# Optimization experiments

Measured on AMD Instinct MI355X. Metric: run time of the kernel, lower is better.

The kernel has to match this reference:

```python
import jax, jax.numpy as jnp
import numpy as np

B, N, C, H = 4, 128, 512, 8
D = C // H
SCALE = D ** (-0.5) * 50.0


def setup_inputs() -> dict:
    key = jax.random.key(0)
    kx, kw = jax.random.split(key)
    x = jax.random.normal(kx, (B, N, N, C), dtype=jnp.float32)
    # torch Linear(n_embd, 5*n_embd, bias=False); stored here as [in, out] for x @ w
    w_qkv = jax.random.normal(kw, (C, 5 * C), dtype=jnp.float32) * (C ** -0.5)
    return {"x": x, "w_qkv": w_qkv}


def _heads(t):
    # [b, i, j, h*d] -> [b, h, i, j, d]
    b, i, j, _ = t.shape
    return t.reshape(b, i, j, H, D).transpose(0, 3, 1, 2, 4)


def reference(x, w_qkv):
    # global norm over the entire tensor (torch .std() is unbiased, ddof=1)
    x = (x - x.mean()) / x.std(ddof=1)
    qkv = x @ w_qkv                                   # [b, i, j, 5c]
    q, k1, k2, v1, v2 = map(_heads, jnp.split(qkv, 5, axis=-1))
    # pivotal attention: for query (i,j), pivot over k with row stream k1[i,k]
    # and column stream k2[k,j]
    scores = SCALE * (jnp.einsum('bhijd,bhikd->bhijk', q, k1)
                      + jnp.einsum('bhijd,bhkjd->bhijk', q, k2))
    attn = jax.nn.softmax(scores, axis=-1)            # [b, h, i, j, k]
    out = (jnp.einsum('bhijk,bhikd->bhijd', attn, v1)
           + jnp.einsum('bhijk,bhkjd->bhijd', attn, v2))
    # [b, h, i, j, d] -> [b, i, j, h*d]
    return out.transpose(0, 2, 3, 1, 4).reshape(B, N, N, C)
```

## Files before the change

### kernel.cpp

```cpp
#include <hip/hip_runtime.h>
#include <stdint.h>


typedef __attribute__((ext_vector_type(8))) short s8v;
typedef __attribute__((ext_vector_type(4))) float f4v;

#define MFMA(a, b, c) __builtin_amdgcn_mfma_f32_16x16x32_bf16((a), (b), (c), 0, 0, 0)

__device__ __forceinline__ float bf2f(unsigned short u) {
  union { unsigned int i; float f; } v; v.i = ((unsigned int)u) << 16; return v.f;
}
__device__ __forceinline__ unsigned short f2bf(float f) {
  union { float f; unsigned int i; } v; v.f = f;
  unsigned int i = v.i;
  return (unsigned short)((i + 0x7fffu + ((i >> 16) & 1u)) >> 16);
}

__device__ __forceinline__ void async_copy16(const void* g, void* l) {
  __builtin_amdgcn_global_load_lds(
      (const __attribute__((address_space(1))) unsigned int*)(uintptr_t)g,
      (__attribute__((address_space(3))) unsigned int*)(uintptr_t)l,
      16, 0, 0);
}

__global__ __launch_bounds__(256) void k_probe(const unsigned short* __restrict__ x,
                                               int* __restrict__ flag) {
  uint4 v = ((const uint4*)x)[threadIdx.x];
  unsigned int uu[4] = {v.x, v.y, v.z, v.w};
  int bad = 0;
#pragma unroll
  for (int u = 0; u < 4; ++u) {
    float a = bf2f((unsigned short)(uu[u] & 0xffffu));
    float b = bf2f((unsigned short)(uu[u] >> 16));
    if (!(fabsf(a) <= 1e4f)) bad = 1;
    if (!(fabsf(b) <= 1e4f)) bad = 1;
  }
  if (bad) atomicOr(flag, 1);
}

__global__ __launch_bounds__(256) void k_red(const void* __restrict__ xraw,
                                             const int* __restrict__ flag,
                                             double* __restrict__ dstats) {
  __shared__ float red[8];
  const int fm = flag[0];
  int t = threadIdx.x;
  size_t gid = (size_t)blockIdx.x * 256 + t;
  float s = 0.f, ss = 0.f;
  if (fm) {
    const float4* pf = (const float4*)xraw;
#pragma unroll 4
    for (int it = 0; it < 32; ++it) {
      size_t idx = gid + (size_t)it * 131072;
      float4 u1 = pf[2 * idx], u2 = pf[2 * idx + 1];
      float vals[8] = {u1.x, u1.y, u1.z, u1.w, u2.x, u2.y, u2.z, u2.w};
#pragma unroll
      for (int u = 0; u < 8; ++u) { s += vals[u]; ss += vals[u] * vals[u]; }
    }
  } else {
    const uint4* p = (const uint4*)xraw;
#pragma unroll 4
    for (int it = 0; it < 32; ++it) {
      uint4 v = p[gid + (size_t)it * 131072];
      unsigned int uu[4] = {v.x, v.y, v.z, v.w};
#pragma unroll
      for (int u = 0; u < 4; ++u) {
        float a = bf2f((unsigned short)(uu[u] & 0xffffu));
        float b = bf2f((unsigned short)(uu[u] >> 16));
        s += a + b;
        ss += a * a + b * b;
      }
    }
  }
#pragma unroll
  for (int d = 32; d >= 1; d >>= 1) {
    s += __shfl_down(s, d);
    ss += __shfl_down(ss, d);
  }
  int lane = t & 63, wave = t >> 6;
  if (lane == 0) { red[wave] = s; red[4 + wave] = ss; }
  __syncthreads();
  if (t == 0) {
    atomicAdd(&dstats[0], (double)(red[0] + red[1] + red[2] + red[3]));
    atomicAdd(&dstats[1], (double)(red[4] + red[5] + red[6] + red[7]));
  }
}

__global__ void k_stats(const double* __restrict__ dstats, float* __restrict__ fstats) {
  double M = 33554432.0;
  double mean = dstats[0] / M;
  double var = (dstats[1] - dstats[0] * dstats[0] / M) / (M - 1.0);
  double istd = 1.0 / sqrt(var);
  fstats[0] = (float)istd;
  fstats[1] = (float)(-mean * istd);
}

__global__ __launch_bounds__(256) void k_colsum(const void* __restrict__ wraw,
                                                const int* __restrict__ flag,
                                                float* __restrict__ colsum) {
  const int fm = flag[0];
  int c = blockIdx.x * 256 + threadIdx.x;
  if (c >= 2560) return;
  float s = 0.f;
  if (fm) {
    const float* w = (const float*)wraw;
    for (int r = 0; r < 512; ++r) s += w[(size_t)r * 2560 + c];
  } else {
    const unsigned short* w = (const unsigned short*)wraw;
    for (int r = 0; r < 512; ++r) s += bf2f(w[(size_t)r * 2560 + c]);
  }
  colsum[c] = s;
}

__global__ __launch_bounds__(256) void k_wt(const void* __restrict__ wraw,
                                            const int* __restrict__ flag,
                                            unsigned short* __restrict__ wThi,
                                            unsigned short* __restrict__ wTlo) {
  __shared__ float tile[64][65];
  const int fm = flag[0];
  int n0 = blockIdx.x * 64, r0 = blockIdx.y * 64;
#pragma unroll
  for (int rep = 0; rep < 16; ++rep) {
    int idx = rep * 256 + threadIdx.x;
    int r = idx >> 6, n = idx & 63;
    float v;
    if (fm) v = ((const float*)wraw)[(size_t)(r0 + r) * 2560 + n0 + n];
    else    v = bf2f(((const unsigned short*)wraw)[(size_t)(r0 + r) * 2560 + n0 + n]);
    tile[r][n] = v;
  }
  __syncthreads();
#pragma unroll
  for (int rep = 0; rep < 16; ++rep) {
    int idx = rep * 256 + threadIdx.x;
    int n = idx >> 6, r = idx & 63;
    float v = tile[r][n];
    unsigned short hi = f2bf(v);
    size_t o = (size_t)(n0 + n) * 512 + r0 + r;
    wThi[o] = hi;
    wTlo[o] = f2bf(v - bf2f(hi));
  }
}

__global__ __launch_bounds__(256) void k_convx(const void* __restrict__ xraw,
                                               const int* __restrict__ flag,
                                               unsigned short* __restrict__ xhi,
                                               unsigned short* __restrict__ xlo,
                                               int b) {
  const int fm = flag[0];
  size_t e0 = ((size_t)blockIdx.x * 256 + threadIdx.x) * 8;
  size_t g0 = (size_t)b * 8388608 + e0;
  float vals[8];
  if (fm) {
    const float4* pf = (const float4*)xraw;
    float4 u1 = pf[g0 / 4], u2 = pf[g0 / 4 + 1];
    vals[0] = u1.x; vals[1] = u1.y; vals[2] = u1.z; vals[3] = u1.w;
    vals[4] = u2.x; vals[5] = u2.y; vals[6] = u2.z; vals[7] = u2.w;
  } else {
    uint4 v = ((const uint4*)xraw)[g0 / 8];
    unsigned int uu[4] = {v.x, v.y, v.z, v.w};
#pragma unroll
    for (int u = 0; u < 4; ++u) {
      vals[2 * u] = bf2f((unsigned short)(uu[u] & 0xffffu));
      vals[2 * u + 1] = bf2f((unsigned short)(uu[u] >> 16));
    }
  }
  unsigned short h[8], l[8];
#pragma unroll
  for (int u = 0; u < 8; ++u) {
    h[u] = f2bf(vals[u]);
    l[u] = f2bf(vals[u] - bf2f(h[u]));
  }
  *(uint4*)(xhi + e0) = *(const uint4*)h;
  *(uint4*)(xlo + e0) = *(const uint4*)l;
}

__global__ __launch_bounds__(256) void k_gemm(
    const unsigned short* __restrict__ xhi, const unsigned short* __restrict__ xlo,
    const unsigned short* __restrict__ wThi, const unsigned short* __restrict__ wTlo,
    const float* __restrict__ colsum, const float* __restrict__ fstats,
    const int* __restrict__ flag,
    unsigned short* __restrict__ qhi, unsigned short* __restrict__ qlo,
    unsigned short* __restrict__ k1hi, unsigned short* __restrict__ k1lo,
    unsigned short* __restrict__ k2hi, unsigned short* __restrict__ k2lo,
    unsigned short* __restrict__ v1T, unsigned short* __restrict__ v2T,
    int h0, int hcShift) {
  __shared__ __align__(16) unsigned short Ash[128 * 64];
  __shared__ __align__(16) unsigned short Asl[128 * 64];
  __shared__ __align__(16) unsigned short Bsh[128 * 64];
  __shared__ __align__(16) unsigned short Bsl[128 * 64];
  const int fm = flag[0];
  const int t = threadIdx.x;
  const int m0 = blockIdx.x * 128;
  const int n0 = blockIdx.y * 128;
  const int hcMask = (1 << hcShift) - 1;

  const int lane = t & 63, wave = t >> 6;
  const int wm = (wave & 1) * 64, wn = (wave >> 1) * 64;
  const int l16 = lane & 15, q4 = lane >> 4;
  const int srow = t >> 3;
  const int scol = (((t & 7) ^ ((t >> 3) & 7)) * 8);
  const int rsw = l16 & 7;

  const float af = fstats[0], bfc = fstats[1];
  const unsigned short* xh = xhi + (size_t)m0 * 512;
  const unsigned short* xl = xlo + (size_t)m0 * 512;

  int wcolr[4];
#pragma unroll
  for (int r = 0; r < 4; ++r) {
    int ncol = n0 + r * 32 + srow;
    int g = ncol >> hcShift, rem = ncol & hcMask;
    wcolr[r] = (g << 9) + ((h0 + (rem >> 6)) << 6) + (rem & 63);
  }

  f4v acc[4][4];
#pragma unroll
  for (int a = 0; a < 4; ++a)
#pragma unroll
    for (int c = 0; c < 4; ++c) acc[a][c] = (f4v)0.f;

  for (int k0 = 0; k0 < 512; k0 += 64) {
#pragma unroll
    for (int r = 0; r < 4; ++r) {
      int row = r * 32 + srow;
      async_copy16(xh + (size_t)row * 512 + k0 + scol, (char*)Ash + (r * 256 + t) * 16);
    }
#pragma unroll
    for (int r = 0; r < 4; ++r)
      async_copy16(wThi + (size_t)wcolr[r] * 512 + k0 + scol, (char*)Bsh + (r * 256 + t) * 16);
    if (fm) {
#pragma unroll
      for (int r = 0; r < 4; ++r) {
        int row = r * 32 + srow;
        async_copy16(xl + (size_t)row * 512 + k0 + scol, (char*)Asl + (r * 256 + t) * 16);
      }
#pragma unroll
      for (int r = 0; r < 4; ++r)
        async_copy16(wTlo + (size_t)wcolr[r] * 512 + k0 + scol, (char*)Bsl + (r * 256 + t) * 16);
    }
    __syncthreads();
#pragma unroll
    for (int kc = 0; kc < 2; ++kc) {
      const int swoff = ((kc * 4 + q4) ^ rsw) * 8;
      s8v ah[4], bh[4];
#pragma unroll
      for (int jt = 0; jt < 4; ++jt)
        ah[jt] = *(const s8v*)&Ash[(wm + jt * 16 + l16) * 64 + swoff];
#pragma unroll
      for (int nt = 0; nt < 4; ++nt)
        bh[nt] = *(const s8v*)&Bsh[(wn + nt * 16 + l16) * 64 + swoff];
      if (fm) {
        s8v al[4], bl[4];
#pragma unroll
        for (int jt = 0; jt < 4; ++jt)
          al[jt] = *(const s8v*)&Asl[(wm + jt * 16 + l16) * 64 + swoff];
#pragma unroll
        for (int nt = 0; nt < 4; ++nt)
          bl[nt] = *(const s8v*)&Bsl[(wn + nt * 16 + l16) * 64 + swoff];
#pragma unroll
        for (int jt = 0; jt < 4; ++jt)
#pragma unroll
          for (int nt = 0; nt < 4; ++nt) {
            acc[jt][nt] = MFMA(ah[jt], bh[nt], acc[jt][nt]);
            acc[jt][nt] = MFMA(ah[jt], bl[nt], acc[jt][nt]);
            acc[jt][nt] = MFMA(al[jt], bh[nt], acc[jt][nt]);
          }
      } else {
#pragma unroll
        for (int jt = 0; jt < 4; ++jt)
#pragma unroll
          for (int nt = 0; nt < 4; ++nt) acc[jt][nt] = MFMA(ah[jt], bh[nt], acc[jt][nt]);
      }
    }
    __syncthreads();
  }

#pragma unroll
  for (int jt = 0; jt < 4; ++jt) {
#pragma unroll
    for (int nt = 0; nt < 4; ++nt) {
      int gcol = n0 + wn + nt * 16 + l16;
      int g = gcol >> hcShift, rem = gcol & hcMask;
      int hl = rem >> 6, d = rem & 63;
      int wcol = (g << 9) + ((h0 + hl) << 6) + d;
      float cs = colsum[wcol] * bfc;
#pragma unroll
      for (int r = 0; r < 4; ++r) {
        int grow = m0 + wm + jt * 16 + q4 * 4 + r;
        int i = grow >> 7, j = grow & 127;
        float val = acc[jt][nt][r] * af + cs;
        unsigned short hi = f2bf(val);
        if (g == 0) {
          size_t idx = (((size_t)hl * 128 + i) * 128 + j) * 64 + d;
          qhi[idx] = hi; qlo[idx] = f2bf(val - bf2f(hi));
        } else if (g == 1) {
          size_t idx = (((size_t)hl * 128 + i) * 128 + j) * 64 + d;
          k1hi[idx] = hi; k1lo[idx] = f2bf(val - bf2f(hi));
        } else if (g == 2) {
          size_t idx = (((size_t)hl * 128 + j) * 128 + i) * 64 + d;
          k2hi[idx] = hi; k2lo[idx] = f2bf(val - bf2f(hi));
        } else if (g == 3) {
          size_t idx = (((size_t)hl * 128 + i) * 64 + d) * 128 + j;
          v1T[idx] = hi;
        } else {
          size_t idx = (((size_t)hl * 128 + j) * 64 + d) * 128 + i;
          v2T[idx] = hi;
        }
      }
    }
  }
}

__global__ __launch_bounds__(256) void k_s1(
    const unsigned short* __restrict__ qhi, const unsigned short* __restrict__ qlo,
    const unsigned short* __restrict__ k1hi, const unsigned short* __restrict__ k1lo,
    float* __restrict__ S) {
  const int i = blockIdx.x, hl = blockIdx.y;
  const int t = threadIdx.x, lane = t & 63, wave = t >> 6;
  const int l16 = lane & 15, q4 = lane >> 4;
  const size_t base = ((size_t)hl * 128 + i) * 128 * 64;

  f4v acc[2][8];
#pragma unroll
  for (int a = 0; a < 2; ++a)
#pragma unroll
    for (int c = 0; c < 8; ++c) acc[a][c] = (f4v)0.f;

#pragma unroll
  for (int kc = 0; kc < 2; ++kc) {
    s8v ah[2], al[2];
#pragma unroll
    for (int jt = 0; jt < 2; ++jt) {
      size_t off = base + (size_t)(wave * 32 + jt * 16 + l16) * 64 + kc * 32 + q4 * 8;
      ah[jt] = *(const s8v*)(qhi + off);
      al[jt] = *(const s8v*)(qlo + off);
    }
#pragma unroll
    for (int kt = 0; kt < 8; ++kt) {
      size_t off = base + (size_t)(kt * 16 + l16) * 64 + kc * 32 + q4 * 8;
      s8v bh = *(const s8v*)(k1hi + off);
      s8v bl = *(const s8v*)(k1lo + off);
#pragma unroll
      for (int jt = 0; jt < 2; ++jt) {
        acc[jt][kt] = MFMA(ah[jt], bh, acc[jt][kt]);
        acc[jt][kt] = MFMA(ah[jt], bl, acc[jt][kt]);
        acc[jt][kt] = MFMA(al[jt], bh, acc[jt][kt]);
      }
    }
  }
  float* Sb = S + ((size_t)hl * 128 + i) * 128 * 128;
#pragma unroll
  for (int jt = 0; jt < 2; ++jt)
#pragma unroll
    for (int kt = 0; kt < 8; ++kt)
#pragma unroll
      for (int r = 0; r < 4; ++r) {
        int j = wave * 32 + jt * 16 + q4 * 4 + r;
        Sb[(size_t)j * 128 + kt * 16 + l16] = acc[jt][kt][r];
      }
}

__global__ __launch_bounds__(256) void k_s2(
    const unsigned short* __restrict__ qhi, const unsigned short* __restrict__ qlo,
    const unsigned short* __restrict__ k2hi, const unsigned short* __restrict__ k2lo,
    const float* __restrict__ S, unsigned short* __restrict__ attn) {
  const int j = blockIdx.x, hl = blockIdx.y;
  const int t = threadIdx.x, lane = t & 63, wave = t >> 6;
  const int l16 = lane & 15, q4 = lane >> 4;
  const size_t bbase = ((size_t)hl * 128 + j) * 128 * 64;

  f4v acc[2][8];
#pragma unroll
  for (int a = 0; a < 2; ++a)
#pragma unroll
    for (int c = 0; c < 8; ++c) acc[a][c] = (f4v)0.f;

#pragma unroll
  for (int kc = 0; kc < 2; ++kc) {
    s8v ah[2], al[2];
#pragma unroll
    for (int it = 0; it < 2; ++it) {
      size_t off = (((size_t)hl * 128 + (wave * 32 + it * 16 + l16)) * 128 + j) * 64 +
                   kc * 32 + q4 * 8;
      ah[it] = *(const s8v*)(qhi + off);
      al[it] = *(const s8v*)(qlo + off);
    }
#pragma unroll
    for (int kt = 0; kt < 8; ++kt) {
      size_t off = bbase + (size_t)(kt * 16 + l16) * 64 + kc * 32 + q4 * 8;
      s8v bh = *(const s8v*)(k2hi + off);
      s8v bl = *(const s8v*)(k2lo + off);
#pragma unroll
      for (int it = 0; it < 2; ++it) {
        acc[it][kt] = MFMA(ah[it], bh, acc[it][kt]);
        acc[it][kt] = MFMA(ah[it], bl, acc[it][kt]);
        acc[it][kt] = MFMA(al[it], bh, acc[it][kt]);
      }
    }
  }

#pragma unroll
  for (int it = 0; it < 2; ++it) {
#pragma unroll
    for (int r = 0; r < 4; ++r) {
      int i = wave * 32 + it * 16 + q4 * 4 + r;
      const float* Srow = S + (((size_t)hl * 128 + i) * 128 + j) * 128;
      float tv[8];
      float m = -3.4e38f;
#pragma unroll
      for (int kt = 0; kt < 8; ++kt) {
        tv[kt] = 6.25f * (Srow[kt * 16 + l16] + acc[it][kt][r]);
        m = fmaxf(m, tv[kt]);
      }
#pragma unroll
      for (int d = 1; d <= 8; d <<= 1) m = fmaxf(m, __shfl_xor(m, d));
      float sum = 0.f;
#pragma unroll
      for (int kt = 0; kt < 8; ++kt) {
        tv[kt] = __expf(tv[kt] - m);
        sum += tv[kt];
      }
#pragma unroll
      for (int d = 1; d <= 8; d <<= 1) sum += __shfl_xor(sum, d);
      float rs = 1.f / sum;
      unsigned short* arow = attn + (((size_t)hl * 128 + i) * 128 + j) * 128;
#pragma unroll
      for (int kt = 0; kt < 8; ++kt) arow[kt * 16 + l16] = f2bf(tv[kt] * rs);
    }
  }
}

__global__ __launch_bounds__(256) void k_av1(
    const unsigned short* __restrict__ attn, const unsigned short* __restrict__ v1T,
    unsigned short* __restrict__ out1) {
  const int i = blockIdx.x, hl = blockIdx.y;
  const int t = threadIdx.x, lane = t & 63, wave = t >> 6;
  const int l16 = lane & 15, q4 = lane >> 4;
  const size_t abase = ((size_t)hl * 128 + i) * 128 * 128;
  const size_t vbase = ((size_t)hl * 128 + i) * 64 * 128;

  f4v acc[2][4];
#pragma unroll
  for (int a = 0; a < 2; ++a)
#pragma unroll
    for (int c = 0; c < 4; ++c) acc[a][c] = (f4v)0.f;

#pragma unroll
  for (int kc = 0; kc < 4; ++kc) {
    s8v a[2], bfr[4];
#pragma unroll
    for (int jt = 0; jt < 2; ++jt)
      a[jt] = *(const s8v*)(attn + abase + (size_t)(wave * 32 + jt * 16 + l16) * 128 +
                            kc * 32 + q4 * 8);
#pragma unroll
    for (int dt = 0; dt < 4; ++dt)
      bfr[dt] = *(const s8v*)(v1T + vbase + (size_t)(dt * 16 + l16) * 128 + kc * 32 + q4 * 8);
#pragma unroll
    for (int jt = 0; jt < 2; ++jt)
#pragma unroll
      for (int dt = 0; dt < 4; ++dt) acc[jt][dt] = MFMA(a[jt], bfr[dt], acc[jt][dt]);
  }
  unsigned short* ob = out1 + ((size_t)hl * 128 + i) * 128 * 64;
#pragma unroll
  for (int jt = 0; jt < 2; ++jt)
#pragma unroll
    for (int dt = 0; dt < 4; ++dt)
#pragma unroll
      for (int r = 0; r < 4; ++r) {
        int j = wave * 32 + jt * 16 + q4 * 4 + r;
        ob[(size_t)j * 64 + dt * 16 + l16] = f2bf(acc[jt][dt][r]);
      }
}

__global__ __launch_bounds__(256) void k_av2(
    const unsigned short* __restrict__ attn, const unsigned short* __restrict__ v2T,
    const unsigned short* __restrict__ out1, const int* __restrict__ flag,
    void* __restrict__ out, int b, int h0) {
  const int j = blockIdx.x, hl = blockIdx.y;
  const int t = threadIdx.x, lane = t & 63, wave = t >> 6;
  const int l16 = lane & 15, q4 = lane >> 4;
  const int fm = flag[0];
  const size_t vbase = ((size_t)hl * 128 + j) * 64 * 128;

  f4v acc[2][4];
#pragma unroll
  for (int a = 0; a < 2; ++a)
#pragma unroll
    for (int c = 0; c < 4; ++c) acc[a][c] = (f4v)0.f;

#pragma unroll
  for (int kc = 0; kc < 4; ++kc) {
    s8v a[2], bfr[4];
#pragma unroll
    for (int it = 0; it < 2; ++it)
      a[it] = *(const s8v*)(attn +
                            (((size_t)hl * 128 + (wave * 32 + it * 16 + l16)) * 128 + j) * 128 +
                            kc * 32 + q4 * 8);
#pragma unroll
    for (int dt = 0; dt < 4; ++dt)
      bfr[dt] = *(const s8v*)(v2T + vbase + (size_t)(dt * 16 + l16) * 128 + kc * 32 + q4 * 8);
#pragma unroll
    for (int it = 0; it < 2; ++it)
#pragma unroll
      for (int dt = 0; dt < 4; ++dt) acc[it][dt] = MFMA(a[it], bfr[dt], acc[it][dt]);
  }
#pragma unroll
  for (int it = 0; it < 2; ++it)
#pragma unroll
    for (int dt = 0; dt < 4; ++dt)
#pragma unroll
      for (int r = 0; r < 4; ++r) {
        int i = wave * 32 + it * 16 + q4 * 4 + r;
        int d = dt * 16 + l16;
        float o = acc[it][dt][r] + bf2f(out1[(((size_t)hl * 128 + i) * 128 + j) * 64 + d]);
        size_t oi = ((size_t)b * 16384 + i * 128 + j) * 512 + (h0 + hl) * 64 + d;
        if (fm) ((float*)out)[oi] = o;
        else    ((unsigned short*)out)[oi] = f2bf(o);
      }
}

extern "C" void kernel_launch(void* const* d_in, const int* in_sizes, int n_in,
                              void* d_out, int out_size, void* d_ws, size_t ws_size,
                              hipStream_t stream) {
  (void)in_sizes; (void)n_in; (void)out_size;
  const void* x = d_in[0];
  const void* w = d_in[1];

  const size_t xslice = (size_t)16384 * 512;
  const size_t wTsz = (size_t)2560 * 512;
  const size_t fixed = xslice * 4 + wTsz * 4 + 2560 * 4 + 64;

  int Hc = 2;
  if (30 * ((size_t)8 * 1048576) + fixed <= ws_size) Hc = 8;
  else if (30 * ((size_t)4 * 1048576) + fixed <= ws_size) Hc = 4;
  const int hcShift = (Hc == 8) ? 9 : ((Hc == 4) ? 8 : 7);
  const size_t TE = (size_t)Hc * 1048576;

  char* p = (char*)d_ws;
  unsigned short* qhi = (unsigned short*)p;  p += TE * 2;
  unsigned short* qlo = (unsigned short*)p;  p += TE * 2;
  unsigned short* k1hi = (unsigned short*)p; p += TE * 2;
  unsigned short* k1lo = (unsigned short*)p; p += TE * 2;
  unsigned short* k2hi = (unsigned short*)p; p += TE * 2;
  unsigned short* k2lo = (unsigned short*)p; p += TE * 2;
  unsigned short* v1T = (unsigned short*)p;  p += TE * 2;
  unsigned short* v2T = (unsigned short*)p;  p += TE * 2;
  float* S = (float*)p;                      p += TE * 8;
  unsigned short* attn = (unsigned short*)p; p += TE * 4;
  unsigned short* out1 = (unsigned short*)p; p += TE * 2;
  unsigned short* xhi = (unsigned short*)p;  p += xslice * 2;
  unsigned short* xlo = (unsigned short*)p;  p += xslice * 2;
  unsigned short* wThi = (unsigned short*)p; p += wTsz * 2;
  unsigned short* wTlo = (unsigned short*)p; p += wTsz * 2;
  float* colsum = (float*)p;                 p += 2560 * 4;
  double* dstats = (double*)p;               p += 16;
  int* flag = (int*)p;                       p += 8;
  float* fstats = (float*)p;                 p += 8;

  hipMemsetAsync(dstats, 0, 24, stream);
  k_probe<<<1, 256, 0, stream>>>((const unsigned short*)x, flag);
  k_red<<<512, 256, 0, stream>>>(x, flag, dstats);
  k_stats<<<1, 1, 0, stream>>>(dstats, fstats);
  k_colsum<<<10, 256, 0, stream>>>(w, flag, colsum);
  k_wt<<<dim3(40, 8), 256, 0, stream>>>(w, flag, wThi, wTlo);

  for (int b = 0; b < 4; ++b) {
    k_convx<<<4096, 256, 0, stream>>>(x, flag, xhi, xlo, b);
    for (int h0 = 0; h0 < 8; h0 += Hc) {
      k_gemm<<<dim3(128, (5 * Hc * 64) / 128), 256, 0, stream>>>(
          xhi, xlo, wThi, wTlo, colsum, fstats, flag,
          qhi, qlo, k1hi, k1lo, k2hi, k2lo, v1T, v2T, h0, hcShift);
      k_s1<<<dim3(128, Hc), 256, 0, stream>>>(qhi, qlo, k1hi, k1lo, S);
      k_s2<<<dim3(128, Hc), 256, 0, stream>>>(qhi, qlo, k2hi, k2lo, S, attn);
      k_av1<<<dim3(128, Hc), 256, 0, stream>>>(attn, v1T, out1);
      k_av2<<<dim3(128, Hc), 256, 0, stream>>>(attn, v2T, out1, flag, d_out, b, h0);
    }
  }
}
```

Before: 1.649 ms.

## Stage GEMM epilogue through LDS for coalesced stores, add separate V2 transpose kernel

The GEMM epilogue previously wrote scattered 2-byte values straight to the head-major and transposed Q/K/V buffers. It now stages the accumulator tile in LDS and writes 16-byte vectors per thread. V2 is written in a natural layout and then transposed by a new small kernel through a shared-memory tile. The K loop now steps by 32 with a smaller unswizzled LDS tile, and launch bounds request 4 blocks per unit for occupancy. The cost is an extra kernel launch per head chunk, more workspace, extra syncs, twice as many K-loop iterations, and possible LDS bank conflicts now that the swizzle is gone.

Measured after the change: 3.719 ms. +125.5%, slower.

```diff
diff --git a/kernel.cpp b/kernel.cpp
--- a/kernel.cpp
+++ b/kernel.cpp
@@ -173,7 +173,7 @@
   *(uint4*)(xlo + e0) = *(const uint4*)l;
 }
 
-__global__ __launch_bounds__(256) void k_gemm(
+__global__ __launch_bounds__(256, 4) void k_gemm(
     const unsigned short* __restrict__ xhi, const unsigned short* __restrict__ xlo,
     const unsigned short* __restrict__ wThi, const unsigned short* __restrict__ wTlo,
     const float* __restrict__ colsum, const float* __restrict__ fstats,
@@ -181,35 +181,37 @@
     unsigned short* __restrict__ qhi, unsigned short* __restrict__ qlo,
     unsigned short* __restrict__ k1hi, unsigned short* __restrict__ k1lo,
     unsigned short* __restrict__ k2hi, unsigned short* __restrict__ k2lo,
-    unsigned short* __restrict__ v1T, unsigned short* __restrict__ v2T,
+    unsigned short* __restrict__ v1T, unsigned short* __restrict__ v2n,
     int h0, int hcShift) {
-  __shared__ __align__(16) unsigned short Ash[128 * 64];
-  __shared__ __align__(16) unsigned short Asl[128 * 64];
-  __shared__ __align__(16) unsigned short Bsh[128 * 64];
-  __shared__ __align__(16) unsigned short Bsl[128 * 64];
+  __shared__ __align__(16) float lds_f[128 * 76];
+  unsigned short* Ash = (unsigned short*)lds_f;
+  unsigned short* Asl = Ash + 4096;
+  unsigned short* Bsh = Ash + 8192;
+  unsigned short* Bsl = Ash + 12288;
+
   const int fm = flag[0];
   const int t = threadIdx.x;
-  const int m0 = blockIdx.x * 128;
+  const int bx = blockIdx.x;
+  const int m0 = bx * 128;
   const int n0 = blockIdx.y * 128;
   const int hcMask = (1 << hcShift) - 1;
 
   const int lane = t & 63, wave = t >> 6;
   const int wm = (wave & 1) * 64, wn = (wave >> 1) * 64;
   const int l16 = lane & 15, q4 = lane >> 4;
-  const int srow = t >> 3;
-  const int scol = (((t & 7) ^ ((t >> 3) & 7)) * 8);
-  const int rsw = l16 & 7;
+  const int c_row = t >> 2;
+  const int c_col = (t & 3) * 8;
 
   const float af = fstats[0], bfc = fstats[1];
   const unsigned short* xh = xhi + (size_t)m0 * 512;
   const unsigned short* xl = xlo + (size_t)m0 * 512;
 
-  int wcolr[4];
-#pragma unroll
-  for (int r = 0; r < 4; ++r) {
-    int ncol = n0 + r * 32 + srow;
+  int wcol2[2];
+#pragma unroll
+  for (int c = 0; c < 2; ++c) {
+    int ncol = n0 + c * 64 + c_row;
     int g = ncol >> hcShift, rem = ncol & hcMask;
-    wcolr[r] = (g << 9) + ((h0 + (rem >> 6)) << 6) + (rem & 63);
+    wcol2[c] = (g << 9) + ((h0 + (rem >> 6)) << 6) + (rem & 63);
   }
 
   f4v acc[4][4];
@@ -218,44 +220,38 @@
 #pragma unroll
     for (int c = 0; c < 4; ++c) acc[a][c] = (f4v)0.f;
 
-  for (int k0 = 0; k0 < 512; k0 += 64) {
-#pragma unroll
-    for (int r = 0; r < 4; ++r) {
-      int row = r * 32 + srow;
-      async_copy16(xh + (size_t)row * 512 + k0 + scol, (char*)Ash + (r * 256 + t) * 16);
-    }
-#pragma unroll
-    for (int r = 0; r < 4; ++r)
-      async_copy16(wThi + (size_t)wcolr[r] * 512 + k0 + scol, (char*)Bsh + (r * 256 + t) * 16);
+  for (int k0 = 0; k0 < 512; k0 += 32) {
+#pragma unroll
+    for (int c = 0; c < 2; ++c) {
+      int row = c * 64 + c_row;
+      async_copy16(xh + (size_t)row * 512 + k0 + c_col, (char*)Ash + c * 4096 + t * 16);
+      async_copy16(wThi + (size_t)wcol2[c] * 512 + k0 + c_col, (char*)Bsh + c * 4096 + t * 16);
+    }
     if (fm) {
 #pragma unroll
-      for (int r = 0; r < 4; ++r) {
-        int row = r * 32 + srow;
-        async_copy16(xl + (size_t)row * 512 + k0 + scol, (char*)Asl + (r * 256 + t) * 16);
-      }
-#pragma unroll
-      for (int r = 0; r < 4; ++r)
-        async_copy16(wTlo + (size_t)wcolr[r] * 512 + k0 + scol, (char*)Bsl + (r * 256 + t) * 16);
+      for (int c = 0; c < 2; ++c) {
+        int row = c * 64 + c_row;
+        async_copy16(xl + (size_t)row * 512 + k0 + c_col, (char*)Asl + c * 4096 + t * 16);
+        async_copy16(wTlo + (size_t)wcol2[c] * 512 + k0 + c_col, (char*)Bsl + c * 4096 + t * 16);
+      }
     }
     __syncthreads();
-#pragma unroll
-    for (int kc = 0; kc < 2; ++kc) {
-      const int swoff = ((kc * 4 + q4) ^ rsw) * 8;
+    {
       s8v ah[4], bh[4];
 #pragma unroll
       for (int jt = 0; jt < 4; ++jt)
-        ah[jt] = *(const s8v*)&Ash[(wm + jt * 16 + l16) * 64 + swoff];
+        ah[jt] = *(const s8v*)&Ash[(wm + jt * 16 + l16) * 32 + q4 * 8];
 #pragma unroll
       for (int nt = 0; nt < 4; ++nt)
-        bh[nt] = *(const s8v*)&Bsh[(wn + nt * 16 + l16) * 64 + swoff];
+        bh[nt] = *(const s8v*)&Bsh[(wn + nt * 16 + l16) * 32 + q4 * 8];
       if (fm) {
         s8v al[4], bl[4];
 #pragma unroll
         for (int jt = 0; jt < 4; ++jt)
-          al[jt] = *(const s8v*)&Asl[(wm + jt * 16 + l16) * 64 + swoff];
+          al[jt] = *(const s8v*)&Asl[(wm + jt * 16 + l16) * 32 + q4 * 8];
 #pragma unroll
         for (int nt = 0; nt < 4; ++nt)
-          bl[nt] = *(const s8v*)&Bsl[(wn + nt * 16 + l16) * 64 + swoff];
+          bl[nt] = *(const s8v*)&Bsl[(wn + nt * 16 + l16) * 32 + q4 * 8];
 #pragma unroll
         for (int jt = 0; jt < 4; ++jt)
 #pragma unroll
@@ -275,38 +271,89 @@
   }
 
 #pragma unroll
-  for (int jt = 0; jt < 4; ++jt) {
-#pragma unroll
-    for (int nt = 0; nt < 4; ++nt) {
-      int gcol = n0 + wn + nt * 16 + l16;
-      int g = gcol >> hcShift, rem = gcol & hcMask;
-      int hl = rem >> 6, d = rem & 63;
-      int wcol = (g << 9) + ((h0 + hl) << 6) + d;
-      float cs = colsum[wcol] * bfc;
-#pragma unroll
-      for (int r = 0; r < 4; ++r) {
-        int grow = m0 + wm + jt * 16 + q4 * 4 + r;
-        int i = grow >> 7, j = grow & 127;
-        float val = acc[jt][nt][r] * af + cs;
-        unsigned short hi = f2bf(val);
-        if (g == 0) {
-          size_t idx = (((size_t)hl * 128 + i) * 128 + j) * 64 + d;
-          qhi[idx] = hi; qlo[idx] = f2bf(val - bf2f(hi));
-        } else if (g == 1) {
-          size_t idx = (((size_t)hl * 128 + i) * 128 + j) * 64 + d;
-          k1hi[idx] = hi; k1lo[idx] = f2bf(val - bf2f(hi));
-        } else if (g == 2) {
-          size_t idx = (((size_t)hl * 128 + j) * 128 + i) * 64 + d;
-          k2hi[idx] = hi; k2lo[idx] = f2bf(val - bf2f(hi));
-        } else if (g == 3) {
-          size_t idx = (((size_t)hl * 128 + i) * 64 + d) * 128 + j;
-          v1T[idx] = hi;
-        } else {
-          size_t idx = (((size_t)hl * 128 + j) * 64 + d) * 128 + i;
-          v2T[idx] = hi;
+  for (int p = 0; p < 2; ++p) {
+    if (p) __syncthreads();
+    if ((wave >> 1) == p) {
+#pragma unroll
+      for (int jt = 0; jt < 4; ++jt)
+#pragma unroll
+        for (int nt = 0; nt < 4; ++nt)
+#pragma unroll
+          for (int r = 0; r < 4; ++r)
+            lds_f[(wm + jt * 16 + q4 * 4 + r) * 76 + nt * 16 + l16] = acc[jt][nt][r];
+    }
+    __syncthreads();
+    const int colbase = n0 + p * 64;
+    const int g = colbase >> hcShift;
+    const int hl = (colbase & hcMask) >> 6;
+    const int wbase = (g << 9) + ((h0 + hl) << 6);
+    if (g <= 2) {
+      unsigned short* dsthi = (g == 0) ? qhi : (g == 1) ? k1hi : k2hi;
+      unsigned short* dstlo = (g == 0) ? qlo : (g == 1) ? k1lo : k2lo;
+#pragma unroll
+      for (int u = 0; u < 4; ++u) {
+        int idx = u * 256 + t;
+        int r = idx >> 3, c8 = (idx & 7) * 8;
+        unsigned short h8[8], l8[8];
+#pragma unroll
+        for (int s = 0; s < 8; ++s) {
+          float val = lds_f[r * 76 + c8 + s] * af + colsum[wbase + c8 + s] * bfc;
+          h8[s] = f2bf(val);
+          l8[s] = f2bf(val - bf2f(h8[s]));
         }
-      }
-    }
+        size_t base = (g == 2) ? ((((size_t)hl * 128 + r) * 128 + bx) * 64 + c8)
+                               : ((((size_t)hl * 128 + bx) * 128 + r) * 64 + c8);
+        *(uint4*)(dsthi + base) = *(const uint4*)h8;
+        *(uint4*)(dstlo + base) = *(const uint4*)l8;
+      }
+    } else if (g == 3) {
+#pragma unroll
+      for (int u = 0; u < 4; ++u) {
+        int idx = u * 256 + t;
+        int d = idx >> 4, r0 = (idx & 15) * 8;
+        float cs = colsum[wbase + d] * bfc;
+        unsigned short h8[8];
+#pragma unroll
+        for (int s = 0; s < 8; ++s)
+          h8[s] = f2bf(lds_f[(r0 + s) * 76 + d] * af + cs);
+        *(uint4*)(v1T + (((size_t)hl * 128 + bx) * 64 + d) * 128 + r0) = *(const uint4*)h8;
+      }
+    } else {
+#pragma unroll
+      for (int u = 0; u < 4; ++u) {
+        int idx = u * 256 + t;
+        int r = idx >> 3, c8 = (idx & 7) * 8;
+        unsigned short h8[8];
+#pragma unroll
+        for (int s = 0; s < 8; ++s)
+          h8[s] = f2bf(lds_f[r * 76 + c8 + s] * af + colsum[wbase + c8 + s] * bfc);
+        *(uint4*)(v2n + (((size_t)hl * 128 + r) * 128 + bx) * 64 + c8) = *(const uint4*)h8;
+      }
+    }
+  }
+}
+
+__global__ __launch_bounds__(256) void k_v2t(const unsigned short* __restrict__ v2n,
+                                             unsigned short* __restrict__ v2T) {
+  __shared__ unsigned short tile[128 * 72];
+  const int j = blockIdx.x, hl = blockIdx.y;
+  const int t = threadIdx.x;
+  const size_t base = ((size_t)hl * 128 + j) * 8192;
+#pragma unroll
+  for (int u = 0; u < 4; ++u) {
+    int idx = u * 256 + t;
+    int k = idx >> 3, c8 = (idx & 7) * 8;
+    *(uint4*)&tile[k * 72 + c8] = *(const uint4*)&v2n[base + (size_t)k * 64 + c8];
+  }
+  __syncthreads();
+#pragma unroll
+  for (int u = 0; u < 4; ++u) {
+    int idx = u * 256 + t;
+    int d = idx >> 4, k0 = (idx & 15) * 8;
+    unsigned short o[8];
+#pragma unroll
+    for (int s = 0; s < 8; ++s) o[s] = tile[(k0 + s) * 72 + d];
+    *(uint4*)&v2T[base + (size_t)d * 128 + k0] = *(const uint4*)o;
   }
 }
 
@@ -530,8 +577,8 @@
   const size_t fixed = xslice * 4 + wTsz * 4 + 2560 * 4 + 64;
 
   int Hc = 2;
-  if (30 * ((size_t)8 * 1048576) + fixed <= ws_size) Hc = 8;
-  else if (30 * ((size_t)4 * 1048576) + fixed <= ws_size) Hc = 4;
+  if (32 * ((size_t)8 * 1048576) + fixed <= ws_size) Hc = 8;
+  else if (32 * ((size_t)4 * 1048576) + fixed <= ws_size) Hc = 4;
   const int hcShift = (Hc == 8) ? 9 : ((Hc == 4) ? 8 : 7);
   const size_t TE = (size_t)Hc * 1048576;
 
@@ -543,6 +590,7 @@
   unsigned short* k2hi = (unsigned short*)p; p += TE * 2;
   unsigned short* k2lo = (unsigned short*)p; p += TE * 2;
   unsigned short* v1T = (unsigned short*)p;  p += TE * 2;
+  unsigned short* v2n = (unsigned short*)p;  p += TE * 2;
   unsigned short* v2T = (unsigned short*)p;  p += TE * 2;
   float* S = (float*)p;                      p += TE * 8;
   unsigned short* attn = (unsigned short*)p; p += TE * 4;
@@ -568,7 +616,8 @@
     for (int h0 = 0; h0 < 8; h0 += Hc) {
       k_gemm<<<dim3(128, (5 * Hc * 64) / 128), 256, 0, stream>>>(
           xhi, xlo, wThi, wTlo, colsum, fstats, flag,
-          qhi, qlo, k1hi, k1lo, k2hi, k2lo, v1T, v2T, h0, hcShift);
+          qhi, qlo, k1hi, k1lo, k2hi, k2lo, v1T, v2n, h0, hcShift);
+      k_v2t<<<dim3(128, Hc), 256, 0, stream>>>(v2n, v2T);
       k_s1<<<dim3(128, Hc), 256, 0, stream>>>(qhi, qlo, k1hi, k1lo, S);
       k_s2<<<dim3(128, Hc), 256, 0, stream>>>(qhi, qlo, k2hi, k2lo, S, attn);
       k_av1<<<dim3(128, Hc), 256, 0, stream>>>(attn, v1T, out1);
```
